# Optimization experiments

Hardware: AMD Instinct MI355X
Metric: run time of the kernel (lower is better)

Reference implementation:

```python
import jax, jax.numpy as jnp
import numpy as np

N_GENE = 100000
N_DIS = 20000
H = 128
E = 500000


def setup_inputs() -> dict:
    key = jax.random.key(0)
    ks = jax.random.split(key, 12)
    s1 = 1.0 / np.sqrt(2 * H)  # fan-in init scale, Linear(2H, H)
    s2 = 1.0 / np.sqrt(H)      # fan-in init scale, Linear(H, 1)
    z_gene = jax.random.normal(ks[0], (N_GENE, H), jnp.float32)
    z_disease = jax.random.normal(ks[1], (N_DIS, H), jnp.float32)
    # gene->disease edges: row indexes genes, col indexes diseases
    edges_gd = jnp.stack([
        jax.random.randint(ks[2], (E,), 0, N_GENE),
        jax.random.randint(ks[3], (E,), 0, N_DIS),
    ])
    # gene->gene edges
    edges_gg = jnp.stack([
        jax.random.randint(ks[4], (E,), 0, N_GENE),
        jax.random.randint(ks[5], (E,), 0, N_GENE),
    ])
    return {
        "z_gene": z_gene,
        "z_disease": z_disease,
        "edges_gd": edges_gd,
        "edges_gg": edges_gg,
        "w1_gd": jax.random.normal(ks[6], (2 * H, H), jnp.float32) * s1,
        "b1_gd": jnp.zeros((H,), jnp.float32),
        "w2_gd": jax.random.normal(ks[7], (H, 1), jnp.float32) * s2,
        "b2_gd": jnp.zeros((1,), jnp.float32),
        "w1_gg": jax.random.normal(ks[8], (2 * H, H), jnp.float32) * s1,
        "b1_gg": jnp.zeros((H,), jnp.float32),
        "w2_gg": jax.random.normal(ks[9], (H, 1), jnp.float32) * s2,
        "b2_gg": jnp.zeros((1,), jnp.float32),
    }


def _decode(z_src, z_dst, edges, w1, b1, w2, b2):
    # gather src/dst node embeddings by edge index, concat -> [E, 2H]
    z = jnp.concatenate([z_src[edges[0]], z_dst[edges[1]]], axis=1)
    h = jnp.maximum(z @ w1 + b1, 0.0)  # Linear + ReLU
    return h @ w2 + b2                  # Linear -> [E, 1]


def reference(z_gene, z_disease, edges_gd, edges_gg,
              w1_gd, b1_gd, w2_gd, b2_gd,
              w1_gg, b1_gg, w2_gg, b2_gg):
    out_gd = _decode(z_gene, z_disease, edges_gd, w1_gd, b1_gd, w2_gd, b2_gd)
    out_gg = _decode(z_gene, z_gene, edges_gg, w1_gg, b1_gg, w2_gg, b2_gg)
    # dict of per-relation outputs in the original; stack since E matches
    return jnp.stack([out_gd, out_gg])  # [2, E, 1]
```

## Files before the change

### kernel.cpp

```cpp
#include <hip/hip_runtime.h>
#include <hip/hip_bf16.h>

#define HDIM 128

typedef __attribute__((ext_vector_type(8))) short short8;
typedef __attribute__((ext_vector_type(4))) float floatx4;

__device__ __forceinline__ float bf2f(unsigned short u) {
    return __uint_as_float(((unsigned)u) << 16);
}
__device__ __forceinline__ unsigned short f2b(float f) {
    __hip_bfloat16 h = __float2bfloat16(f);
    return __builtin_bit_cast(unsigned short, h);
}
__device__ __forceinline__ float ldv(const void* p, size_t i, int flag) {
    return flag ? bf2f(((const unsigned short*)p)[i]) : ((const float*)p)[i];
}
__device__ __forceinline__ short8 pack8(float4 a, float4 b) {
    short8 r;
    r[0] = (short)f2b(a.x); r[1] = (short)f2b(a.y);
    r[2] = (short)f2b(a.z); r[3] = (short)f2b(a.w);
    r[4] = (short)f2b(b.x); r[5] = (short)f2b(b.y);
    r[6] = (short)f2b(b.z); r[7] = (short)f2b(b.w);
    return r;
}

__device__ __forceinline__ int local_detect(const unsigned short* zbits) {
    __shared__ int red[256];
    int tid = threadIdx.x;
    int cnt = 0;
    for (int i = tid; i < 4096; i += 256) {
        int ex = (zbits[i] >> 7) & 0xFF;
        if (ex >= 100 && ex <= 140) cnt++;
    }
    red[tid] = cnt;
    __syncthreads();
    for (int s = 128; s > 0; s >>= 1) {
        if (tid < s) red[tid] += red[tid + s];
        __syncthreads();
    }
    return (red[0] >= 3686) ? 1 : 0;
}

__global__ __launch_bounds__(256) void prep_kernel(
    const unsigned short* __restrict__ zbits,
    const void* __restrict__ w1_gd, const void* __restrict__ w1_gg,
    const void* __restrict__ b1_gd, const void* __restrict__ w2_gd,
    const void* __restrict__ b2_gd, const void* __restrict__ b1_gg,
    const void* __restrict__ w2_gg, const void* __restrict__ b2_gg,
    unsigned short* __restrict__ img, float* __restrict__ params,
    int* __restrict__ flagout)
{
    int flag = local_detect(zbits);
    int b = blockIdx.x;
    int tid = threadIdx.x;
    if (b < 32) {
        int im   = b >> 3;
        int sub  = b & 7;
        const void* w1 = (im < 2) ? w1_gd : w1_gg;
        int part = im & 1;
        unsigned short* out = img + im * 16384;
        int n = tid & 127;
#pragma unroll
        for (int it = 0; it < 8; ++it) {
            int k = sub * 16 + it * 2 + (tid >> 7);
            unsigned short v = flag
                ? ((const unsigned short*)w1)[(size_t)(part * 128 + k) * 128 + n]
                : f2b(((const float*)w1)[(size_t)(part * 128 + k) * 128 + n]);
            out[n * 128 + (((k >> 3) ^ (n & 15)) << 3) + (k & 7)] = v;
        }
    } else {
        if (tid < 128) {
            params[tid]       = ldv(b1_gd, tid, flag);
            params[256 + tid] = ldv(b1_gg, tid, flag);
            params[768 + tid] = 0.f;
        } else {
            params[tid]       = ldv(w2_gd, tid - 128, flag);
            params[256 + tid] = ldv(w2_gg, tid - 128, flag);
        }
        if (tid == 0) {
            params[512] = ldv(b2_gd, 0, flag);
            params[513] = ldv(b2_gg, 0, flag);
            *flagout = flag;
        }
    }
}

__global__ __launch_bounds__(256) void proj_kernel(
    const void* __restrict__ Zg, const void* __restrict__ Zd,
    const uint4* __restrict__ img, const float* __restrict__ params,
    unsigned short* __restrict__ A_gd, unsigned short* __restrict__ B_gd,
    unsigned short* __restrict__ A_gg, unsigned short* __restrict__ B_gg,
    int NG, int ND, int gblk, const int* __restrict__ flagp)
{
    __shared__ uint4 sW[2048];
    int id = blockIdx.x;
    const void* Z; int M; const uint4* W; unsigned short* Out; const float* bias;
    if (id < gblk)            { Z = Zg; M = NG; W = img;            Out = A_gd; bias = params;       }
    else if (id < 2 * gblk)   { Z = Zg; M = NG; W = img + 2 * 2048; Out = A_gg; bias = params + 256; id -= gblk; }
    else if (id < 3 * gblk)   { Z = Zg; M = NG; W = img + 3 * 2048; Out = B_gg; bias = params + 768; id -= 2 * gblk; }
    else                      { Z = Zd; M = ND; W = img + 2048;     Out = B_gd; bias = params + 768; id -= 3 * gblk; }

    int tid  = threadIdx.x;
    int lane = tid & 63;
    int wave = tid >> 6;
    int nl   = lane & 15;
    int quad = lane >> 4;

#pragma unroll
    for (int i = 0; i < 8; ++i) sW[tid + i * 256] = W[tid + i * 256];

    int row0 = id * 128 + wave * 32 + nl;
    int row1 = row0 + 16;
    int r0c = row0 < M ? row0 : (M - 1);
    int r1c = row1 < M ? row1 : (M - 1);

    short8 zf[2][4];
    if (*flagp) {
        const uint4* z0 = (const uint4*)Z + (size_t)r0c * 16;
        const uint4* z1 = (const uint4*)Z + (size_t)r1c * 16;
#pragma unroll
        for (int kc = 0; kc < 4; ++kc) {
            zf[0][kc] = __builtin_bit_cast(short8, z0[kc * 4 + quad]);
            zf[1][kc] = __builtin_bit_cast(short8, z1[kc * 4 + quad]);
        }
    } else {
        const float4* z0 = (const float4*)Z + (size_t)r0c * 32;
        const float4* z1 = (const float4*)Z + (size_t)r1c * 32;
#pragma unroll
        for (int kc = 0; kc < 4; ++kc) {
            int o = kc * 8 + quad * 2;
            zf[0][kc] = pack8(z0[o], z0[o + 1]);
            zf[1][kc] = pack8(z1[o], z1[o + 1]);
        }
    }
    __syncthreads();

    floatx4 acc[2][8];
#pragma unroll
    for (int rt = 0; rt < 2; ++rt)
#pragma unroll
        for (int nt = 0; nt < 8; ++nt)
            acc[rt][nt] = (floatx4){0.f, 0.f, 0.f, 0.f};

#pragma unroll
    for (int kc = 0; kc < 4; ++kc) {
        int p = (kc * 4 + quad) ^ nl;
#pragma unroll
        for (int nt = 0; nt < 8; ++nt) {
            short8 wf = __builtin_bit_cast(short8, sW[(nt * 16 + nl) * 16 + p]);
            acc[0][nt] = __builtin_amdgcn_mfma_f32_16x16x32_bf16(wf, zf[0][kc], acc[0][nt], 0, 0, 0);
            acc[1][nt] = __builtin_amdgcn_mfma_f32_16x16x32_bf16(wf, zf[1][kc], acc[1][nt], 0, 0, 0);
        }
    }

#pragma unroll
    for (int rt = 0; rt < 2; ++rt) {
        int row = rt ? row1 : row0;
        if (row < M) {
#pragma unroll
            for (int nt = 0; nt < 8; ++nt) {
                float4 bv = *(const float4*)(bias + nt * 16 + quad * 4);
                ushort4 v;
                v.x = f2b(acc[rt][nt][0] + bv.x);
                v.y = f2b(acc[rt][nt][1] + bv.y);
                v.z = f2b(acc[rt][nt][2] + bv.z);
                v.w = f2b(acc[rt][nt][3] + bv.w);
                *(ushort4*)(Out + (size_t)row * HDIM + nt * 16 + quad * 4) = v;
            }
        }
    }
}

__global__ __launch_bounds__(256) void edge_kernel(
    const int* __restrict__ edges_gd, const int* __restrict__ edges_gg,
    const unsigned short* __restrict__ A_gd, const unsigned short* __restrict__ B_gd,
    const unsigned short* __restrict__ A_gg, const unsigned short* __restrict__ B_gg,
    const float* __restrict__ params,
    void* __restrict__ out, int E, int nb, const int* __restrict__ flagp)
{
    int rel = ((int)blockIdx.x >= nb) ? 1 : 0;
    int blk = blockIdx.x - rel * nb;
    const int* edges = rel ? edges_gg : edges_gd;
    const unsigned short* A = rel ? A_gg : A_gd;
    const unsigned short* B = rel ? B_gg : B_gd;
    const float* w2 = params + 128 + rel * 256;
    float b2 = params[512 + rel];

    int tid  = threadIdx.x;
    int lane = tid & 63;
    int wave = tid >> 6;
    int nl   = lane & 7;
    int grp  = lane >> 3;

    float w2f[16];
#pragma unroll
    for (int i = 0; i < 4; ++i) {
        float4 t = *(const float4*)(w2 + nl * 16 + i * 4);
        w2f[i * 4 + 0] = t.x; w2f[i * 4 + 1] = t.y;
        w2f[i * 4 + 2] = t.z; w2f[i * 4 + 3] = t.w;
    }

    int e0 = blk * 128 + (wave * 8 + grp) * 4;
    int ecap = E - 4;
    int ec = e0 < ecap ? e0 : ecap;
    int4 sp = *(const int4*)(edges + ec);
    int4 dp = *(const int4*)(edges + E + ec);
    int s0 = sp.x, s1 = sp.y, s2 = sp.z, s3 = sp.w;
    int d0 = dp.x, d1 = dp.y, d2 = dp.z, d3 = dp.w;
    if (e0 != ec) {
        s0 = (e0 + 0 < E) ? edges[e0 + 0] : s0;  d0 = (e0 + 0 < E) ? edges[E + e0 + 0] : d0;
        s1 = (e0 + 1 < E) ? edges[e0 + 1] : s1;  d1 = (e0 + 1 < E) ? edges[E + e0 + 1] : d1;
        s2 = (e0 + 2 < E) ? edges[e0 + 2] : s2;  d2 = (e0 + 2 < E) ? edges[E + e0 + 2] : d2;
        s3 = (e0 + 3 < E) ? edges[e0 + 3] : s3;  d3 = (e0 + 3 < E) ? edges[E + e0 + 3] : d3;
    }

    const uint4* ap0 = (const uint4*)(A + (size_t)s0 * HDIM) + nl * 2;
    const uint4* bp0 = (const uint4*)(B + (size_t)d0 * HDIM) + nl * 2;
    const uint4* ap1 = (const uint4*)(A + (size_t)s1 * HDIM) + nl * 2;
    const uint4* bp1 = (const uint4*)(B + (size_t)d1 * HDIM) + nl * 2;
    const uint4* ap2 = (const uint4*)(A + (size_t)s2 * HDIM) + nl * 2;
    const uint4* bp2 = (const uint4*)(B + (size_t)d2 * HDIM) + nl * 2;
    const uint4* ap3 = (const uint4*)(A + (size_t)s3 * HDIM) + nl * 2;
    const uint4* bp3 = (const uint4*)(B + (size_t)d3 * HDIM) + nl * 2;

    uint4 a[4][2], c[4][2];
    a[0][0] = ap0[0]; a[0][1] = ap0[1]; c[0][0] = bp0[0]; c[0][1] = bp0[1];
    a[1][0] = ap1[0]; a[1][1] = ap1[1]; c[1][0] = bp1[0]; c[1][1] = bp1[1];
    a[2][0] = ap2[0]; a[2][1] = ap2[1]; c[2][0] = bp2[0]; c[2][1] = bp2[1];
    a[3][0] = ap3[0]; a[3][1] = ap3[1]; c[3][0] = bp3[0]; c[3][1] = bp3[1];

    float acc[4] = {0.f, 0.f, 0.f, 0.f};
#pragma unroll
    for (int k = 0; k < 4; ++k) {
#pragma unroll
        for (int i = 0; i < 2; ++i) {
            const unsigned* au = (const unsigned*)&a[k][i];
            const unsigned* cu = (const unsigned*)&c[k][i];
#pragma unroll
            for (int j = 0; j < 4; ++j) {
                int ch = i * 8 + j * 2;
                float x0 = __uint_as_float(au[j] << 16);
                float x1 = __uint_as_float(au[j] & 0xffff0000u);
                float y0 = __uint_as_float(cu[j] << 16);
                float y1 = __uint_as_float(cu[j] & 0xffff0000u);
                acc[k] = fmaf(fmaxf(x0 + y0, 0.f), w2f[ch], acc[k]);
                acc[k] = fmaf(fmaxf(x1 + y1, 0.f), w2f[ch + 1], acc[k]);
            }
        }
    }
#pragma unroll
    for (int k = 0; k < 4; ++k) {
        acc[k] += __shfl_xor(acc[k], 1);
        acc[k] += __shfl_xor(acc[k], 2);
        acc[k] += __shfl_xor(acc[k], 4);
    }

    if (nl == 0) {
        int flag = *flagp;
        size_t base = (size_t)rel * E;
        float r0 = acc[0] + b2, r1 = acc[1] + b2, r2 = acc[2] + b2, r3 = acc[3] + b2;
        if (e0 + 3 < E) {
            if (flag) {
                ushort4 v = {f2b(r0), f2b(r1), f2b(r2), f2b(r3)};
                *(ushort4*)((unsigned short*)out + base + e0) = v;
            } else {
                float4 v = {r0, r1, r2, r3};
                *(float4*)((float*)out + base + e0) = v;
            }
        } else {
            float rr[4] = {r0, r1, r2, r3};
#pragma unroll
            for (int k = 0; k < 4; ++k) {
                if (e0 + k < E) {
                    if (flag) ((unsigned short*)out)[base + e0 + k] = f2b(rr[k]);
                    else      ((float*)out)[base + e0 + k] = rr[k];
                }
            }
        }
    }
}

__global__ __launch_bounds__(256) void detect_kernel(
    const unsigned short* __restrict__ zbits, int* __restrict__ flag)
{
    int f = local_detect(zbits);
    if (threadIdx.x == 0) *flag = f;
}

__global__ __launch_bounds__(128) void naive_edge_kernel(
    const int* __restrict__ edges,
    const void* __restrict__ zsrc, const void* __restrict__ zdst,
    const void* __restrict__ w1, const void* __restrict__ b1,
    const void* __restrict__ w2, const void* __restrict__ b2,
    void* __restrict__ out, size_t eoff, int E,
    const int* __restrict__ flagp)
{
    int flag = flagp ? *flagp : 0;
    __shared__ float zs[128], zd[128], red[128];
    int e = blockIdx.x;
    int n = threadIdx.x;
    int src = edges[e], dst = edges[E + e];
    zs[n] = ldv(zsrc, (size_t)src * HDIM + n, flag);
    zd[n] = ldv(zdst, (size_t)dst * HDIM + n, flag);
    __syncthreads();
    float acc = ldv(b1, n, flag);
    for (int k = 0; k < 128; ++k) acc = fmaf(zs[k], ldv(w1, (size_t)k * HDIM + n, flag), acc);
    for (int k = 0; k < 128; ++k) acc = fmaf(zd[k], ldv(w1, (size_t)(128 + k) * HDIM + n, flag), acc);
    red[n] = fmaxf(acc, 0.f) * ldv(w2, n, flag);
    __syncthreads();
    for (int s = 64; s > 0; s >>= 1) {
        if (n < s) red[n] += red[n + s];
        __syncthreads();
    }
    if (n == 0) {
        float r = red[0] + ldv(b2, 0, flag);
        if (flag) ((unsigned short*)out)[eoff + e] = f2b(r);
        else      ((float*)out)[eoff + e] = r;
    }
}

extern "C" void kernel_launch(void* const* d_in, const int* in_sizes, int n_in,
                              void* d_out, int out_size, void* d_ws, size_t ws_size,
                              hipStream_t stream)
{
    const void* z_gene = d_in[0];
    const void* z_dis  = d_in[1];
    const int* edges_gd = (const int*)d_in[2];
    const int* edges_gg = (const int*)d_in[3];
    const void* w1_gd = d_in[4];
    const void* b1_gd = d_in[5];
    const void* w2_gd = d_in[6];
    const void* b2_gd = d_in[7];
    const void* w1_gg = d_in[8];
    const void* b1_gg = d_in[9];
    const void* w2_gg = d_in[10];
    const void* b2_gg = d_in[11];

    int NG = in_sizes[0] / HDIM;
    int ND = in_sizes[1] / HDIM;
    int E  = in_sizes[2] / 2;

    size_t off_flag   = 0;
    size_t off_params = 256;
    size_t off_img    = 256 + 4096;
    size_t off_Agd    = off_img + 131072;
    size_t off_Bgd    = off_Agd + (size_t)NG * HDIM * 2;
    size_t off_Agg    = off_Bgd + (size_t)ND * HDIM * 2;
    size_t off_Bgg    = off_Agg + (size_t)NG * HDIM * 2;
    size_t need       = off_Bgg + (size_t)NG * HDIM * 2;

    char* ws = (char*)d_ws;

    if (ws_size < need) {
        const int* flagp = nullptr;
        if (ws_size >= 16) {
            detect_kernel<<<1, 256, 0, stream>>>((const unsigned short*)z_gene, (int*)ws);
            flagp = (const int*)ws;
        }
        naive_edge_kernel<<<E, 128, 0, stream>>>(edges_gd, z_gene, z_dis,
                                                 w1_gd, b1_gd, w2_gd, b2_gd,
                                                 d_out, 0, E, flagp);
        naive_edge_kernel<<<E, 128, 0, stream>>>(edges_gg, z_gene, z_gene,
                                                 w1_gg, b1_gg, w2_gg, b2_gg,
                                                 d_out, (size_t)E, E, flagp);
        return;
    }

    int* flag = (int*)(ws + off_flag);
    float* params = (float*)(ws + off_params);
    unsigned short* img = (unsigned short*)(ws + off_img);
    unsigned short* Agd = (unsigned short*)(ws + off_Agd);
    unsigned short* Bgd = (unsigned short*)(ws + off_Bgd);
    unsigned short* Agg = (unsigned short*)(ws + off_Agg);
    unsigned short* Bgg = (unsigned short*)(ws + off_Bgg);

    prep_kernel<<<33, 256, 0, stream>>>((const unsigned short*)z_gene,
                                        w1_gd, w1_gg, b1_gd, w2_gd, b2_gd,
                                        b1_gg, w2_gg, b2_gg, img, params, flag);

    const uint4* img4 = (const uint4*)img;
    int gblk = (NG + 127) / 128;
    int dblk = (ND + 127) / 128;
    proj_kernel<<<3 * gblk + dblk, 256, 0, stream>>>(z_gene, z_dis, img4, params,
                                                     Agd, Bgd, Agg, Bgg,
                                                     NG, ND, gblk, flag);

    int nb = (E + 127) / 128;
    edge_kernel<<<2 * nb, 256, 0, stream>>>(edges_gd, edges_gg, Agd, Bgd, Agg, Bgg,
                                            params, d_out, E, nb, flag);
}
```

Before: 229.6 us.

## Use persistent grid-stride loops with prefetch in projection and edge kernels

The projection kernel changes to a fixed grid (160 blocks per gene projection, 32 for disease). Each block now stages the weight image in LDS once and loops over row tiles, prefetching the next tile's rows while running the MFMAs for the current one. The edge kernel likewise becomes a persistent 1024-block grid-stride loop that prefetches the next group's edge indices during the gather and compute. This is meant to amortize weight staging and launch overhead and to hide load latency, at the cost of fewer resident waves and more register pressure.

```diff
diff --git a/kernel.cpp b/kernel.cpp
--- a/kernel.cpp
+++ b/kernel.cpp
@@ -2,6 +2,9 @@
 #include <hip/hip_bf16.h>
 
 #define HDIM 128
+#define PGB 160
+#define PDB 32
+#define ENB 512
 
 typedef __attribute__((ext_vector_type(8))) short short8;
 typedef __attribute__((ext_vector_type(4))) float floatx4;
@@ -86,20 +89,125 @@
     }
 }
 
+template<bool BF16>
+__device__ __forceinline__ void load_raw(const void* __restrict__ Z, int t, int M,
+                                         int wave, int nl, int quad, uint4* raw)
+{
+    int row0 = t * 128 + wave * 32 + nl;
+    int row1 = row0 + 16;
+    int r0 = row0 < M ? row0 : M - 1;
+    int r1 = row1 < M ? row1 : M - 1;
+    if (BF16) {
+        const uint4* z0 = (const uint4*)Z + (size_t)r0 * 16;
+        const uint4* z1 = (const uint4*)Z + (size_t)r1 * 16;
+#pragma unroll
+        for (int kc = 0; kc < 4; ++kc) {
+            raw[kc]     = z0[kc * 4 + quad];
+            raw[4 + kc] = z1[kc * 4 + quad];
+        }
+    } else {
+        const uint4* z0 = (const uint4*)Z + (size_t)r0 * 32;
+        const uint4* z1 = (const uint4*)Z + (size_t)r1 * 32;
+#pragma unroll
+        for (int kc = 0; kc < 4; ++kc) {
+            int o = kc * 8 + quad * 2;
+            raw[2 * kc]         = z0[o];
+            raw[2 * kc + 1]     = z0[o + 1];
+            raw[8 + 2 * kc]     = z1[o];
+            raw[8 + 2 * kc + 1] = z1[o + 1];
+        }
+    }
+}
+
+template<bool BF16>
+__device__ __forceinline__ void to_frags(const uint4* raw, short8 zf[2][4])
+{
+#pragma unroll
+    for (int kc = 0; kc < 4; ++kc) {
+        if (BF16) {
+            zf[0][kc] = __builtin_bit_cast(short8, raw[kc]);
+            zf[1][kc] = __builtin_bit_cast(short8, raw[4 + kc]);
+        } else {
+            zf[0][kc] = pack8(__builtin_bit_cast(float4, raw[2 * kc]),
+                              __builtin_bit_cast(float4, raw[2 * kc + 1]));
+            zf[1][kc] = pack8(__builtin_bit_cast(float4, raw[8 + 2 * kc]),
+                              __builtin_bit_cast(float4, raw[8 + 2 * kc + 1]));
+        }
+    }
+}
+
+template<bool BF16>
+__device__ void proj_loop(const void* __restrict__ Z,
+                          unsigned short* __restrict__ Out,
+                          const float* __restrict__ bias,
+                          const uint4* sW, int M, int ntiles,
+                          int t0, int nb, int wave, int nl, int quad)
+{
+    constexpr int NR = BF16 ? 8 : 16;
+    uint4 raw[NR];
+    int t = t0;
+    if (t < ntiles) load_raw<BF16>(Z, t, M, wave, nl, quad, raw);
+    while (t < ntiles) {
+        short8 zf[2][4];
+        to_frags<BF16>(raw, zf);
+
+        int tn = t + nb;
+        if (tn < ntiles) load_raw<BF16>(Z, tn, M, wave, nl, quad, raw);
+
+        floatx4 acc[2][8];
+#pragma unroll
+        for (int rt = 0; rt < 2; ++rt)
+#pragma unroll
+            for (int nt = 0; nt < 8; ++nt)
+                acc[rt][nt] = (floatx4){0.f, 0.f, 0.f, 0.f};
+
+#pragma unroll
+        for (int kc = 0; kc < 4; ++kc) {
+            int p = (kc * 4 + quad) ^ nl;
+#pragma unroll
+            for (int nt = 0; nt < 8; ++nt) {
+                short8 wf = __builtin_bit_cast(short8, sW[(nt * 16 + nl) * 16 + p]);
+                acc[0][nt] = __builtin_amdgcn_mfma_f32_16x16x32_bf16(wf, zf[0][kc], acc[0][nt], 0, 0, 0);
+                acc[1][nt] = __builtin_amdgcn_mfma_f32_16x16x32_bf16(wf, zf[1][kc], acc[1][nt], 0, 0, 0);
+            }
+        }
+
+        int row0 = t * 128 + wave * 32 + nl;
+#pragma unroll
+        for (int rt = 0; rt < 2; ++rt) {
+            int row = row0 + rt * 16;
+            if (row < M) {
+#pragma unroll
+                for (int nt = 0; nt < 8; ++nt) {
+                    float4 bv = *(const float4*)(bias + nt * 16 + quad * 4);
+                    ushort4 v;
+                    v.x = f2b(acc[rt][nt][0] + bv.x);
+                    v.y = f2b(acc[rt][nt][1] + bv.y);
+                    v.z = f2b(acc[rt][nt][2] + bv.z);
+                    v.w = f2b(acc[rt][nt][3] + bv.w);
+                    *(ushort4*)(Out + (size_t)row * HDIM + nt * 16 + quad * 4) = v;
+                }
+            }
+        }
+        t = tn;
+    }
+}
+
 __global__ __launch_bounds__(256) void proj_kernel(
     const void* __restrict__ Zg, const void* __restrict__ Zd,
     const uint4* __restrict__ img, const float* __restrict__ params,
     unsigned short* __restrict__ A_gd, unsigned short* __restrict__ B_gd,
     unsigned short* __restrict__ A_gg, unsigned short* __restrict__ B_gg,
-    int NG, int ND, int gblk, const int* __restrict__ flagp)
+    int NG, int ND, const int* __restrict__ flagp)
 {
     __shared__ uint4 sW[2048];
     int id = blockIdx.x;
     const void* Z; int M; const uint4* W; unsigned short* Out; const float* bias;
-    if (id < gblk)            { Z = Zg; M = NG; W = img;            Out = A_gd; bias = params;       }
-    else if (id < 2 * gblk)   { Z = Zg; M = NG; W = img + 2 * 2048; Out = A_gg; bias = params + 256; id -= gblk; }
-    else if (id < 3 * gblk)   { Z = Zg; M = NG; W = img + 3 * 2048; Out = B_gg; bias = params + 768; id -= 2 * gblk; }
-    else                      { Z = Zd; M = ND; W = img + 2048;     Out = B_gd; bias = params + 768; id -= 3 * gblk; }
+    int lblk, nb;
+    if (id < PGB)            { Z = Zg; M = NG; W = img;        Out = A_gd; bias = params;       lblk = id;           nb = PGB; }
+    else if (id < 2 * PGB)   { Z = Zg; M = NG; W = img + 4096; Out = A_gg; bias = params + 256; lblk = id - PGB;     nb = PGB; }
+    else if (id < 3 * PGB)   { Z = Zg; M = NG; W = img + 6144; Out = B_gg; bias = params + 768; lblk = id - 2 * PGB; nb = PGB; }
+    else                     { Z = Zd; M = ND; W = img + 2048; Out = B_gd; bias = params + 768; lblk = id - 3 * PGB; nb = PDB; }
 
     int tid  = threadIdx.x;
     int lane = tid & 63;
@@ -109,67 +217,11 @@
 
 #pragma unroll
     for (int i = 0; i < 8; ++i) sW[tid + i * 256] = W[tid + i * 256];
-
-    int row0 = id * 128 + wave * 32 + nl;
-    int row1 = row0 + 16;
-    int r0c = row0 < M ? row0 : (M - 1);
-    int r1c = row1 < M ? row1 : (M - 1);
-
-    short8 zf[2][4];
-    if (*flagp) {
-        const uint4* z0 = (const uint4*)Z + (size_t)r0c * 16;
-        const uint4* z1 = (const uint4*)Z + (size_t)r1c * 16;
-#pragma unroll
-        for (int kc = 0; kc < 4; ++kc) {
-            zf[0][kc] = __builtin_bit_cast(short8, z0[kc * 4 + quad]);
-            zf[1][kc] = __builtin_bit_cast(short8, z1[kc * 4 + quad]);
-        }
-    } else {
-        const float4* z0 = (const float4*)Z + (size_t)r0c * 32;
-        const float4* z1 = (const float4*)Z + (size_t)r1c * 32;
-#pragma unroll
-        for (int kc = 0; kc < 4; ++kc) {
-            int o = kc * 8 + quad * 2;
-            zf[0][kc] = pack8(z0[o], z0[o + 1]);
-            zf[1][kc] = pack8(z1[o], z1[o + 1]);
-        }
-    }
     __syncthreads();
 
-    floatx4 acc[2][8];
-#pragma unroll
-    for (int rt = 0; rt < 2; ++rt)
-#pragma unroll
-        for (int nt = 0; nt < 8; ++nt)
-            acc[rt][nt] = (floatx4){0.f, 0.f, 0.f, 0.f};
-
-#pragma unroll
-    for (int kc = 0; kc < 4; ++kc) {
-        int p = (kc * 4 + quad) ^ nl;
-#pragma unroll
-        for (int nt = 0; nt < 8; ++nt) {
-            short8 wf = __builtin_bit_cast(short8, sW[(nt * 16 + nl) * 16 + p]);
-            acc[0][nt] = __builtin_amdgcn_mfma_f32_16x16x32_bf16(wf, zf[0][kc], acc[0][nt], 0, 0, 0);
-            acc[1][nt] = __builtin_amdgcn_mfma_f32_16x16x32_bf16(wf, zf[1][kc], acc[1][nt], 0, 0, 0);
-        }
-    }
-
-#pragma unroll
-    for (int rt = 0; rt < 2; ++rt) {
-        int row = rt ? row1 : row0;
-        if (row < M) {
-#pragma unroll
-            for (int nt = 0; nt < 8; ++nt) {
-                float4 bv = *(const float4*)(bias + nt * 16 + quad * 4);
-                ushort4 v;
-                v.x = f2b(acc[rt][nt][0] + bv.x);
-                v.y = f2b(acc[rt][nt][1] + bv.y);
-                v.z = f2b(acc[rt][nt][2] + bv.z);
-                v.w = f2b(acc[rt][nt][3] + bv.w);
-                *(ushort4*)(Out + (size_t)row * HDIM + nt * 16 + quad * 4) = v;
-            }
-        }
-    }
+    int ntiles = (M + 127) >> 7;
+    if (*flagp) proj_loop<true >(Z, Out, bias, sW, M, ntiles, lblk, nb, wave, nl, quad);
+    else        proj_loop<false>(Z, Out, bias, sW, M, ntiles, lblk, nb, wave, nl, quad);
 }
 
 __global__ __launch_bounds__(256) void edge_kernel(
@@ -177,15 +229,16 @@
     const unsigned short* __restrict__ A_gd, const unsigned short* __restrict__ B_gd,
     const unsigned short* __restrict__ A_gg, const unsigned short* __restrict__ B_gg,
     const float* __restrict__ params,
-    void* __restrict__ out, int E, int nb, const int* __restrict__ flagp)
-{
-    int rel = ((int)blockIdx.x >= nb) ? 1 : 0;
-    int blk = blockIdx.x - rel * nb;
+    void* __restrict__ out, int E, const int* __restrict__ flagp)
+{
+    int rel = ((int)blockIdx.x >= ENB) ? 1 : 0;
+    int blk = blockIdx.x - rel * ENB;
     const int* edges = rel ? edges_gg : edges_gd;
     const unsigned short* A = rel ? A_gg : A_gd;
     const unsigned short* B = rel ? B_gg : B_gd;
     const float* w2 = params + 128 + rel * 256;
     float b2 = params[512 + rel];
+    int flag = *flagp;
 
     int tid  = threadIdx.x;
     int lane = tid & 63;
@@ -201,83 +254,100 @@
         w2f[i * 4 + 2] = t.z; w2f[i * 4 + 3] = t.w;
     }
 
-    int e0 = blk * 128 + (wave * 8 + grp) * 4;
-    int ecap = E - 4;
-    int ec = e0 < ecap ? e0 : ecap;
-    int4 sp = *(const int4*)(edges + ec);
-    int4 dp = *(const int4*)(edges + E + ec);
-    int s0 = sp.x, s1 = sp.y, s2 = sp.z, s3 = sp.w;
-    int d0 = dp.x, d1 = dp.y, d2 = dp.z, d3 = dp.w;
-    if (e0 != ec) {
-        s0 = (e0 + 0 < E) ? edges[e0 + 0] : s0;  d0 = (e0 + 0 < E) ? edges[E + e0 + 0] : d0;
-        s1 = (e0 + 1 < E) ? edges[e0 + 1] : s1;  d1 = (e0 + 1 < E) ? edges[E + e0 + 1] : d1;
-        s2 = (e0 + 2 < E) ? edges[e0 + 2] : s2;  d2 = (e0 + 2 < E) ? edges[E + e0 + 2] : d2;
-        s3 = (e0 + 3 < E) ? edges[e0 + 3] : s3;  d3 = (e0 + 3 < E) ? edges[E + e0 + 3] : d3;
-    }
-
-    const uint4* ap0 = (const uint4*)(A + (size_t)s0 * HDIM) + nl * 2;
-    const uint4* bp0 = (const uint4*)(B + (size_t)d0 * HDIM) + nl * 2;
-    const uint4* ap1 = (const uint4*)(A + (size_t)s1 * HDIM) + nl * 2;
-    const uint4* bp1 = (const uint4*)(B + (size_t)d1 * HDIM) + nl * 2;
-    const uint4* ap2 = (const uint4*)(A + (size_t)s2 * HDIM) + nl * 2;
-    const uint4* bp2 = (const uint4*)(B + (size_t)d2 * HDIM) + nl * 2;
-    const uint4* ap3 = (const uint4*)(A + (size_t)s3 * HDIM) + nl * 2;
-    const uint4* bp3 = (const uint4*)(B + (size_t)d3 * HDIM) + nl * 2;
-
-    uint4 a[4][2], c[4][2];
-    a[0][0] = ap0[0]; a[0][1] = ap0[1]; c[0][0] = bp0[0]; c[0][1] = bp0[1];
-    a[1][0] = ap1[0]; a[1][1] = ap1[1]; c[1][0] = bp1[0]; c[1][1] = bp1[1];
-    a[2][0] = ap2[0]; a[2][1] = ap2[1]; c[2][0] = bp2[0]; c[2][1] = bp2[1];
-    a[3][0] = ap3[0]; a[3][1] = ap3[1]; c[3][0] = bp3[0]; c[3][1] = bp3[1];
-
-    float acc[4] = {0.f, 0.f, 0.f, 0.f};
-#pragma unroll
-    for (int k = 0; k < 4; ++k) {
-#pragma unroll
-        for (int i = 0; i < 2; ++i) {
-            const unsigned* au = (const unsigned*)&a[k][i];
-            const unsigned* cu = (const unsigned*)&c[k][i];
-#pragma unroll
-            for (int j = 0; j < 4; ++j) {
-                int ch = i * 8 + j * 2;
-                float x0 = __uint_as_float(au[j] << 16);
-                float x1 = __uint_as_float(au[j] & 0xffff0000u);
-                float y0 = __uint_as_float(cu[j] << 16);
-                float y1 = __uint_as_float(cu[j] & 0xffff0000u);
-                acc[k] = fmaf(fmaxf(x0 + y0, 0.f), w2f[ch], acc[k]);
-                acc[k] = fmaf(fmaxf(x1 + y1, 0.f), w2f[ch + 1], acc[k]);
-            }
-        }
-    }
-#pragma unroll
-    for (int k = 0; k < 4; ++k) {
-        acc[k] += __shfl_xor(acc[k], 1);
-        acc[k] += __shfl_xor(acc[k], 2);
-        acc[k] += __shfl_xor(acc[k], 4);
-    }
-
-    if (nl == 0) {
-        int flag = *flagp;
-        size_t base = (size_t)rel * E;
-        float r0 = acc[0] + b2, r1 = acc[1] + b2, r2 = acc[2] + b2, r3 = acc[3] + b2;
-        if (e0 + 3 < E) {
-            if (flag) {
-                ushort4 v = {f2b(r0), f2b(r1), f2b(r2), f2b(r3)};
-                *(ushort4*)((unsigned short*)out + base + e0) = v;
-            } else {
-                float4 v = {r0, r1, r2, r3};
-                *(float4*)((float*)out + base + e0) = v;
-            }
-        } else {
-            float rr[4] = {r0, r1, r2, r3};
-#pragma unroll
-            for (int k = 0; k < 4; ++k) {
-                if (e0 + k < E) {
-                    if (flag) ((unsigned short*)out)[base + e0 + k] = f2b(rr[k]);
-                    else      ((float*)out)[base + e0 + k] = rr[k];
+    int ngroups = (E + 3) >> 2;
+    int ecap = (E - 4) & ~3;
+    int stride = ENB * 32;
+    int g = blk * 32 + wave * 8 + grp;
+    size_t obase = (size_t)rel * E;
+
+    int4 sp, dp;
+    if (g < ngroups) {
+        int ec = 4 * g; if (ec > ecap) ec = ecap;
+        sp = *(const int4*)(edges + ec);
+        dp = *(const int4*)(edges + E + ec);
+    }
+    while (g < ngroups) {
+        int e0 = 4 * g;
+        int ec = e0 > ecap ? ecap : e0;
+        int s0 = sp.x, s1 = sp.y, s2 = sp.z, s3 = sp.w;
+        int d0 = dp.x, d1 = dp.y, d2 = dp.z, d3 = dp.w;
+        if (e0 != ec) {
+            s0 = (e0 + 0 < E) ? edges[e0 + 0] : s0;  d0 = (e0 + 0 < E) ? edges[E + e0 + 0] : d0;
+            s1 = (e0 + 1 < E) ? edges[e0 + 1] : s1;  d1 = (e0 + 1 < E) ? edges[E + e0 + 1] : d1;
+            s2 = (e0 + 2 < E) ? edges[e0 + 2] : s2;  d2 = (e0 + 2 < E) ? edges[E + e0 + 2] : d2;
+            s3 = (e0 + 3 < E) ? edges[e0 + 3] : s3;  d3 = (e0 + 3 < E) ? edges[E + e0 + 3] : d3;
+        }
+
+        const uint4* ap0 = (const uint4*)(A + (size_t)s0 * HDIM) + nl * 2;
+        const uint4* bp0 = (const uint4*)(B + (size_t)d0 * HDIM) + nl * 2;
+        const uint4* ap1 = (const uint4*)(A + (size_t)s1 * HDIM) + nl * 2;
+        const uint4* bp1 = (const uint4*)(B + (size_t)d1 * HDIM) + nl * 2;
+        const uint4* ap2 = (const uint4*)(A + (size_t)s2 * HDIM) + nl * 2;
+        const uint4* bp2 = (const uint4*)(B + (size_t)d2 * HDIM) + nl * 2;
+        const uint4* ap3 = (const uint4*)(A + (size_t)s3 * HDIM) + nl * 2;
+        const uint4* bp3 = (const uint4*)(B + (size_t)d3 * HDIM) + nl * 2;
+
+        uint4 a[4][2], c[4][2];
+        a[0][0] = ap0[0]; a[0][1] = ap0[1]; c[0][0] = bp0[0]; c[0][1] = bp0[1];
+        a[1][0] = ap1[0]; a[1][1] = ap1[1]; c[1][0] = bp1[0]; c[1][1] = bp1[1];
+        a[2][0] = ap2[0]; a[2][1] = ap2[1]; c[2][0] = bp2[0]; c[2][1] = bp2[1];
+        a[3][0] = ap3[0]; a[3][1] = ap3[1]; c[3][0] = bp3[0]; c[3][1] = bp3[1];
+
+        int gn = g + stride;
+        if (gn < ngroups) {
+            int ecn = 4 * gn; if (ecn > ecap) ecn = ecap;
+            sp = *(const int4*)(edges + ecn);
+            dp = *(const int4*)(edges + E + ecn);
+        }
+
+        float acc[4] = {0.f, 0.f, 0.f, 0.f};
+#pragma unroll
+        for (int k = 0; k < 4; ++k) {
+#pragma unroll
+            for (int i = 0; i < 2; ++i) {
+                const unsigned* au = (const unsigned*)&a[k][i];
+                const unsigned* cu = (const unsigned*)&c[k][i];
+#pragma unroll
+                for (int j = 0; j < 4; ++j) {
+                    int ch = i * 8 + j * 2;
+                    float x0 = __uint_as_float(au[j] << 16);
+                    float x1 = __uint_as_float(au[j] & 0xffff0000u);
+                    float y0 = __uint_as_float(cu[j] << 16);
+                    float y1 = __uint_as_float(cu[j] & 0xffff0000u);
+                    acc[k] = fmaf(fmaxf(x0 + y0, 0.f), w2f[ch], acc[k]);
+                    acc[k] = fmaf(fmaxf(x1 + y1, 0.f), w2f[ch + 1], acc[k]);
                 }
             }
         }
+#pragma unroll
+        for (int k = 0; k < 4; ++k) {
+            acc[k] += __shfl_xor(acc[k], 1);
+            acc[k] += __shfl_xor(acc[k], 2);
+            acc[k] += __shfl_xor(acc[k], 4);
+        }
+
+        if (nl == 0) {
+            float r0 = acc[0] + b2, r1 = acc[1] + b2, r2 = acc[2] + b2, r3 = acc[3] + b2;
+            if (e0 == ec && e0 + 3 < E) {
+                if (flag) {
+                    ushort4 v = {f2b(r0), f2b(r1), f2b(r2), f2b(r3)};
+                    *(ushort4*)((unsigned short*)out + obase + e0) = v;
+                } else {
+                    float4 v = {r0, r1, r2, r3};
+                    *(float4*)((float*)out + obase + e0) = v;
+                }
+            } else {
+                float rr[4] = {r0, r1, r2, r3};
+#pragma unroll
+                for (int k = 0; k < 4; ++k) {
+                    if (e0 + k < E) {
+                        if (flag) ((unsigned short*)out)[obase + e0 + k] = f2b(rr[k]);
+                        else      ((float*)out)[obase + e0 + k] = rr[k];
+                    }
+                }
+            }
+        }
+        g = gn;
     }
 }
 
@@ -380,13 +450,10 @@
                                         b1_gg, w2_gg, b2_gg, img, params, flag);
 
     const uint4* img4 = (const uint4*)img;
-    int gblk = (NG + 127) / 128;
-    int dblk = (ND + 127) / 128;
-    proj_kernel<<<3 * gblk + dblk, 256, 0, stream>>>(z_gene, z_dis, img4, params,
-                                                     Agd, Bgd, Agg, Bgg,
-                                                     NG, ND, gblk, flag);
-
-    int nb = (E + 127) / 128;
-    edge_kernel<<<2 * nb, 256, 0, stream>>>(edges_gd, edges_gg, Agd, Bgd, Agg, Bgg,
-                                            params, d_out, E, nb, flag);
-}
+    proj_kernel<<<3 * PGB + PDB, 256, 0, stream>>>(z_gene, z_dis, img4, params,
+                                                   Agd, Bgd, Agg, Bgg,
+                                                   NG, ND, flag);
+
+    edge_kernel<<<2 * ENB, 256, 0, stream>>>(edges_gd, edges_gg, Agd, Bgd, Agg, Bgg,
+                                             params, d_out, E, flag);
+}
```

Result: slower. 236.1 us (+2.8%).
